# Kernel optimization log

Measured on AMD Instinct MI355X. Metric: run time of the kernel, lower is better.

Reference implementation:

```python
import jax, jax.numpy as jnp
import numpy as np

PAD_INDEX = 0

def setup_inputs() -> dict:
    key = jax.random.key(0)
    k1, k2, k3, k4, k5 = jax.random.split(key, 5)
    B, S, V = 256, 4096, 30
    mlm_outputs = jax.random.normal(k1, (B, S, V), dtype=jnp.float32)
    nsp_outputs = jax.random.normal(k2, (B, 2), dtype=jnp.float32)
    mutation_matrix = jax.random.uniform(k3, (V, V), dtype=jnp.float32)
    mlm_targets = jax.random.randint(k4, (B, S), 0, V, dtype=jnp.int64 if jax.config.jax_enable_x64 else jnp.int32)
    is_nexts = jax.random.randint(k5, (B,), 0, 2, dtype=jnp.int64 if jax.config.jax_enable_x64 else jnp.int32)
    return {
        "mlm_outputs": mlm_outputs,
        "nsp_outputs": nsp_outputs,
        "mutation_matrix": mutation_matrix,
        "mlm_targets": mlm_targets,
        "is_nexts": is_nexts,
    }

def _mutation_ce_loss(logits_flat, targets_flat, mutation_matrix):
    # Faithful to MutaionCrossEntropyLoss: per-sample F.cross_entropy with
    # weight=mutation_matrix[target] and reduction='mean'. For a single sample
    # the weighted mean is (w[t]*nll)/w[t] == nll (weight cancels exactly when
    # w[t] > 0, which holds for the uniform-(0,1) matrix). Ignored (PAD) samples
    # contribute 0; the accumulated sum is divided by total n (including pads).
    n = logits_flat.shape[0]
    logp = jax.nn.log_softmax(logits_flat, axis=-1)            # [N, V]
    nll = -jnp.take_along_axis(logp, targets_flat[:, None], axis=-1)[:, 0]  # [N]
    mask = targets_flat != PAD_INDEX
    return jnp.sum(jnp.where(mask, nll, 0.0)) / n

def reference(mlm_outputs, nsp_outputs, mutation_matrix, mlm_targets, is_nexts):
    B, S, V = mlm_outputs.shape
    mlm_predictions = jnp.argmax(mlm_outputs, axis=2)   # [B, S]
    nsp_predictions = jnp.argmax(nsp_outputs, axis=1)   # [B]
    logits_flat = mlm_outputs.reshape(B * S, V)
    targets_flat = mlm_targets.reshape(B * S)
    mlm_loss = _mutation_ce_loss(logits_flat, targets_flat, mutation_matrix)
    # nsp_loss is computed in the original but unused (loss = mlm_loss)
    loss = mlm_loss[None]  # unsqueeze(dim=0)
    return (mlm_predictions, nsp_predictions, loss)
```

## Files before the change

kernel.cpp:

```cpp
#include <hip/hip_runtime.h>
#include <math.h>

#define B_DIM 256
#define S_DIM 4096
#define V_DIM 30
#define BS_TOTAL (B_DIM * S_DIM)
#define POS_PER_BLOCK 512
#define THREADS 256
#define F4_PER_TILE ((POS_PER_BLOCK * V_DIM) / 4)
#define F4_ITERS (F4_PER_TILE / THREADS)

__global__ __launch_bounds__(THREADS) void mlm_main_kernel(
    const float* __restrict__ logits,
    const int*   __restrict__ targets,
    float*       __restrict__ preds,
    float*       __restrict__ acc)
{
    __shared__ float tile[POS_PER_BLOCK * V_DIM];
    __shared__ float wave_sums[THREADS / 64];

    const int t = threadIdx.x;
    const long long base_pos = (long long)blockIdx.x * POS_PER_BLOCK;

    const float4* gsrc  = (const float4*)(logits + base_pos * V_DIM);
    float4*       ltile = (float4*)tile;
#pragma unroll
    for (int k = 0; k < F4_ITERS; ++k) {
        ltile[t + k * THREADS] = gsrc[t + k * THREADS];
    }
    __syncthreads();

    float local_nll = 0.0f;
#pragma unroll
    for (int p = 0; p < POS_PER_BLOCK / THREADS; ++p) {
        const int pos = t + p * THREADS;
        const float* row = &tile[pos * V_DIM];

        float best = row[0];
        int   bidx = 0;
#pragma unroll
        for (int j = 1; j < V_DIM; ++j) {
            float x = row[j];
            if (x > best) { best = x; bidx = j; }
        }

        float s = 0.0f;
#pragma unroll
        for (int j = 0; j < V_DIM; ++j) {
            s += __expf(row[j] - best);
        }

        const long long gpos = base_pos + pos;
        const int tgt = targets[gpos];
        if (tgt != 0) {
            local_nll += __logf(s) + best - row[tgt];
        }
        preds[gpos] = (float)bidx;
    }

#pragma unroll
    for (int off = 32; off > 0; off >>= 1) {
        local_nll += __shfl_down(local_nll, off, 64);
    }
    const int wid  = t >> 6;
    const int lane = t & 63;
    if (lane == 0) wave_sums[wid] = local_nll;
    __syncthreads();
    if (t == 0) {
        float blk = 0.0f;
#pragma unroll
        for (int w = 0; w < THREADS / 64; ++w) blk += wave_sums[w];
        atomicAdd(acc, blk);
    }
}

__global__ __launch_bounds__(B_DIM) void finalize_kernel(
    const float* __restrict__ nsp,
    const float* __restrict__ acc,
    float*       __restrict__ out_nsp,
    float*       __restrict__ out_loss)
{
    const int b = threadIdx.x;
    const float a0 = nsp[b * 2 + 0];
    const float a1 = nsp[b * 2 + 1];
    out_nsp[b] = (a1 > a0) ? 1.0f : 0.0f;
    if (b == 0) {
        out_loss[0] = acc[0] / (float)BS_TOTAL;
    }
}

extern "C" void kernel_launch(void* const* d_in, const int* in_sizes, int n_in,
                              void* d_out, int out_size, void* d_ws, size_t ws_size,
                              hipStream_t stream) {
    const float* mlm     = (const float*)d_in[0];
    const float* nsp     = (const float*)d_in[1];
    const int*   targets = (const int*)  d_in[3];

    float* out      = (float*)d_out;
    float* preds    = out;
    float* out_nsp  = out + BS_TOTAL;
    float* out_loss = out + BS_TOTAL + B_DIM;

    float* acc = (float*)d_ws;
    hipMemsetAsync(acc, 0, sizeof(float), stream);

    const int grid = BS_TOTAL / POS_PER_BLOCK;
    mlm_main_kernel<<<grid, THREADS, 0, stream>>>(mlm, targets, preds, acc);
    finalize_kernel<<<1, B_DIM, 0, stream>>>(nsp, acc, out_nsp, out_loss);
}
```

Before: 199.0 us.

## Replace global atomic with per-block partials and halve positions per block

Each block now handles 256 positions, one per thread, instead of 512, which doubles the grid and reduces shared memory per block so more blocks fit per CU. Logits are loaded into registers with float2 reads, and the target logit is chosen by a predicated select instead of a dynamic shared-memory index. The single global atomicAdd and its memset are replaced by per-block partial sums that the finalize kernel reduces deterministically. The cost is more blocks to launch and a larger reduction in the finalize kernel.

```diff
diff --git a/kernel.cpp b/kernel.cpp
--- a/kernel.cpp
+++ b/kernel.cpp
@@ -5,87 +5,107 @@
 #define S_DIM 4096
 #define V_DIM 30
 #define BS_TOTAL (B_DIM * S_DIM)
-#define POS_PER_BLOCK 512
+#define POS_PER_BLOCK 256
 #define THREADS 256
+#define GRID (BS_TOTAL / POS_PER_BLOCK)
 #define F4_PER_TILE ((POS_PER_BLOCK * V_DIM) / 4)
-#define F4_ITERS (F4_PER_TILE / THREADS)
 
 __global__ __launch_bounds__(THREADS) void mlm_main_kernel(
     const float* __restrict__ logits,
     const int*   __restrict__ targets,
     float*       __restrict__ preds,
-    float*       __restrict__ acc)
+    float*       __restrict__ partials)
 {
     __shared__ float tile[POS_PER_BLOCK * V_DIM];
     __shared__ float wave_sums[THREADS / 64];
 
     const int t = threadIdx.x;
-    const long long base_pos = (long long)blockIdx.x * POS_PER_BLOCK;
+    const int base_pos = blockIdx.x * POS_PER_BLOCK;
 
-    const float4* gsrc  = (const float4*)(logits + base_pos * V_DIM);
+    const float4* gsrc  = (const float4*)(logits + (size_t)base_pos * V_DIM);
     float4*       ltile = (float4*)tile;
 #pragma unroll
-    for (int k = 0; k < F4_ITERS; ++k) {
+    for (int k = 0; k < 7; ++k) {
         ltile[t + k * THREADS] = gsrc[t + k * THREADS];
+    }
+    if (t < F4_PER_TILE - 7 * THREADS) {
+        ltile[t + 7 * THREADS] = gsrc[t + 7 * THREADS];
     }
     __syncthreads();
 
-    float local_nll = 0.0f;
+    float vals[V_DIM];
+    const float2* row2 = (const float2*)(tile + t * V_DIM);
 #pragma unroll
-    for (int p = 0; p < POS_PER_BLOCK / THREADS; ++p) {
-        const int pos = t + p * THREADS;
-        const float* row = &tile[pos * V_DIM];
-
-        float best = row[0];
-        int   bidx = 0;
-#pragma unroll
-        for (int j = 1; j < V_DIM; ++j) {
-            float x = row[j];
-            if (x > best) { best = x; bidx = j; }
-        }
-
-        float s = 0.0f;
-#pragma unroll
-        for (int j = 0; j < V_DIM; ++j) {
-            s += __expf(row[j] - best);
-        }
-
-        const long long gpos = base_pos + pos;
-        const int tgt = targets[gpos];
-        if (tgt != 0) {
-            local_nll += __logf(s) + best - row[tgt];
-        }
-        preds[gpos] = (float)bidx;
+    for (int j = 0; j < V_DIM / 2; ++j) {
+        const float2 u = row2[j];
+        vals[2 * j]     = u.x;
+        vals[2 * j + 1] = u.y;
     }
 
+    float best = vals[0];
+    int   bidx = 0;
+#pragma unroll
+    for (int j = 1; j < V_DIM; ++j) {
+        if (vals[j] > best) { best = vals[j]; bidx = j; }
+    }
+
+    float s = 0.0f;
+#pragma unroll
+    for (int j = 0; j < V_DIM; ++j) {
+        s += __expf(vals[j] - best);
+    }
+
+    const int gpos = base_pos + t;
+    const int tgt  = targets[gpos];
+
+    float tv = 0.0f;
+#pragma unroll
+    for (int j = 0; j < V_DIM; ++j) {
+        tv = (j == tgt) ? vals[j] : tv;
+    }
+
+    const float nll = (tgt != 0) ? (__logf(s) + best - tv) : 0.0f;
+    preds[gpos] = (float)bidx;
+
+    float r = nll;
 #pragma unroll
     for (int off = 32; off > 0; off >>= 1) {
-        local_nll += __shfl_down(local_nll, off, 64);
+        r += __shfl_down(r, off, 64);
     }
-    const int wid  = t >> 6;
-    const int lane = t & 63;
-    if (lane == 0) wave_sums[wid] = local_nll;
+    if ((t & 63) == 0) wave_sums[t >> 6] = r;
     __syncthreads();
     if (t == 0) {
-        float blk = 0.0f;
-#pragma unroll
-        for (int w = 0; w < THREADS / 64; ++w) blk += wave_sums[w];
-        atomicAdd(acc, blk);
+        partials[blockIdx.x] =
+            wave_sums[0] + wave_sums[1] + wave_sums[2] + wave_sums[3];
     }
 }
 
-__global__ __launch_bounds__(B_DIM) void finalize_kernel(
+__global__ __launch_bounds__(256) void finalize_kernel(
     const float* __restrict__ nsp,
-    const float* __restrict__ acc,
+    const float* __restrict__ partials,
     float*       __restrict__ out_nsp,
     float*       __restrict__ out_loss)
 {
-    const int b = threadIdx.x;
-    const float a0 = nsp[b * 2 + 0];
-    const float a1 = nsp[b * 2 + 1];
-    out_nsp[b] = (a1 > a0) ? 1.0f : 0.0f;
-    if (b == 0) {
-        out_loss[0] = acc[0] / (float)BS_TOTAL;
+    const int t = threadIdx.x;
+
+    const float a0 = nsp[2 * t + 0];
+    const float a1 = nsp[2 * t + 1];
+    out_nsp[t] = (a1 > a0) ? 1.0f : 0.0f;
+
+    float s = 0.0f;
+#pragma unroll
+    for (int i = 0; i < GRID / 256; ++i) {
+        s += partials[t + i * 256];
+    }
+#pragma unroll
+    for (int off = 32; off > 0; off >>= 1) {
+        s += __shfl_down(s, off, 64);
+    }
+    __shared__ float ws[4];
+    if ((t & 63) == 0) ws[t >> 6] = s;
+    __syncthreads();
+    if (t == 0) {
+        out_loss[0] = (ws[0] + ws[1] + ws[2] + ws[3]) / (float)BS_TOTAL;
     }
 }
 
@@ -101,10 +121,8 @@
     float* out_nsp  = out + BS_TOTAL;
     float* out_loss = out + BS_TOTAL + B_DIM;
 
-    float* acc = (float*)d_ws;
-    hipMemsetAsync(acc, 0, sizeof(float), stream);
+    float* partials = (float*)d_ws;
 
-    const int grid = BS_TOTAL / POS_PER_BLOCK;
-    mlm_main_kernel<<<grid, THREADS, 0, stream>>>(mlm, targets, preds, acc);
-    finalize_kernel<<<1, B_DIM, 0, stream>>>(nsp, acc, out_nsp, out_loss);
+    mlm_main_kernel<<<GRID, THREADS, 0, stream>>>(mlm, targets, preds, partials);
+    finalize_kernel<<<1, 256, 0, stream>>>(nsp, partials, out_nsp, out_loss);
 }
```

Result: faster. 193.2 us (-2.9%).
